# Performance work log

Measured on AMD Instinct MI355X. Metric: run time of the kernel, lower is better.

Reference implementation:

```python
import jax, jax.numpy as jnp
import numpy as np

B, T, D, H = 2, 4096, 768, 12
DH = D // H


def setup_inputs() -> dict:
    key = jax.random.key(0)
    ks = jax.random.split(key, 4)
    x = jax.random.normal(ks[0], (B, T, D), dtype=jnp.float32)
    Wqkv = jax.random.normal(ks[1], (D, 3 * D), dtype=jnp.float32) * (D ** -0.5)
    bqkv = jnp.zeros((3 * D,), dtype=jnp.float32)
    Wproj = jax.random.normal(ks[2], (D, D), dtype=jnp.float32) * (D ** -0.5)
    bproj = jnp.zeros((D,), dtype=jnp.float32)
    return {"x": x, "Wqkv": Wqkv, "bqkv": bqkv, "Wproj": Wproj, "bproj": bproj}


def reference(x, Wqkv, bqkv, Wproj, bproj):
    b, t, c = x.shape
    qkv = x @ Wqkv + bqkv                      # [B,T,3D]
    qkv = qkv.reshape(b, t, H, 3 * DH)
    q, k, v = jnp.split(qkv, 3, axis=-1)       # each [B,T,H,DH]
    q = q.transpose(0, 2, 1, 3)                # [B,H,T,DH]
    k = k.transpose(0, 2, 1, 3)
    v = v.transpose(0, 2, 1, 3)
    att = jnp.einsum('bhqd,bhkd->bhqk', q, k) / (DH ** 0.5)  # [B,H,T,T]
    mask = jnp.tril(jnp.ones((t, t), dtype=bool))
    att = jnp.where(mask, att, jnp.float32(-1e9))
    att = jax.nn.softmax(att, axis=-1)
    out = jnp.einsum('bhqk,bhkd->bhqd', att, v)  # [B,H,T,DH]
    out = out.transpose(0, 2, 1, 3).reshape(b, t, c)
    return out @ Wproj + bproj
```

## Files before the change

kernel.cpp:

```cpp
#include <hip/hip_runtime.h>

typedef unsigned short u16;
typedef unsigned int u32;
typedef __bf16 bf16x8 __attribute__((ext_vector_type(8)));
typedef float f32x4 __attribute__((ext_vector_type(4)));
typedef float f32x16 __attribute__((ext_vector_type(16)));
typedef u16 u16x4 __attribute__((ext_vector_type(4)));
typedef u32 u32x2 __attribute__((ext_vector_type(2)));
typedef u32 u32x4 __attribute__((ext_vector_type(4)));

#define QSCALE 0.18033688011112042f

static __device__ __forceinline__ u16 f2bf(float f) {
  __bf16 h = (__bf16)f;
  return __builtin_bit_cast(u16, h);
}

static __device__ __forceinline__ u32 pk2(float a, float b) {
  return (u32)f2bf(a) | ((u32)f2bf(b) << 16);
}

static __device__ __forceinline__ void gl_lds16(const void* g, void* l) {
  __builtin_amdgcn_global_load_lds(
      (const __attribute__((address_space(1))) unsigned int*)g,
      (__attribute__((address_space(3))) unsigned int*)l, 16, 0, 0);
}

static __device__ __forceinline__ void wait_vmcnt0() {
  asm volatile("s_waitcnt vmcnt(0)" ::: "memory");
  __builtin_amdgcn_sched_barrier(0);
}
static __device__ __forceinline__ void barrier_mem() {
  asm volatile("s_barrier" ::: "memory");
  __builtin_amdgcn_sched_barrier(0);
}

static __device__ __forceinline__ f32x16 zero16() {
  f32x16 z;
#pragma unroll
  for (int i = 0; i < 16; ++i) z[i] = 0.f;
  return z;
}

__global__ void k_cvt(const float* __restrict__ in, u16* __restrict__ out, int n4) {
  int i = blockIdx.x * 256 + threadIdx.x;
  if (i < n4) {
    f32x4 f = ((const f32x4*)in)[i];
    u16x4 u = { f2bf(f[0]), f2bf(f[1]), f2bf(f[2]), f2bf(f[3]) };
    ((u16x4*)out)[i] = u;
  }
}

__global__ void k_transpose_cvt(const float* __restrict__ in, u16* __restrict__ out,
                                int R, int C) {
  __shared__ float tile[32][33];
  const int c0 = blockIdx.x * 32, r0 = blockIdx.y * 32;
  const int tx = threadIdx.x, ty = threadIdx.y;
#pragma unroll
  for (int i = 0; i < 4; ++i)
    tile[ty + i * 8][tx] = in[(size_t)(r0 + ty + i * 8) * C + c0 + tx];
  __syncthreads();
#pragma unroll
  for (int i = 0; i < 4; ++i)
    out[(size_t)(c0 + ty + i * 8) * R + r0 + tx] = f2bf(tile[tx][ty + i * 8]);
}

static __device__ __forceinline__ void gemm_core(const u16* __restrict__ Ag,
                                                 const u16* __restrict__ Btg,
                                                 int K, int m0, int n0,
                                                 u16* As, u16* Bs,
                                                 f32x4 acc[4][4]) {
  const int tid = threadIdx.x;
  const int lane = tid & 63;
  const int wid = tid >> 6;
  const int wm = wid >> 1, wn = wid & 1;
  const int l16 = lane & 15, lg = lane >> 4;

  for (int kt = 0; kt < K; kt += 64) {
    __syncthreads();
#pragma unroll
    for (int i = 0; i < 4; ++i) {
      int chunk = i * 256 + tid;
      int row = chunk >> 3;
      int lcb = ((chunk & 7) << 4) ^ ((row & 7) << 4);
      gl_lds16(Ag + (size_t)(m0 + row) * K + kt + (lcb >> 1),
               As + ((i * 256 + wid * 64) << 3));
    }
#pragma unroll
    for (int i = 0; i < 4; ++i) {
      int chunk = i * 256 + tid;
      int row = chunk >> 3;
      int lcb = ((chunk & 7) << 4) ^ ((row & 7) << 4);
      gl_lds16(Btg + (size_t)(n0 + row) * K + kt + (lcb >> 1),
               Bs + ((i * 256 + wid * 64) << 3));
    }
    __syncthreads();

#pragma unroll
    for (int ks = 0; ks < 2; ++ks) {
      bf16x8 af[4], bfr[4];
#pragma unroll
      for (int mi = 0; mi < 4; ++mi) {
        int row = wm * 64 + mi * 16 + l16;
        int off = row * 128 + ((ks * 64 + (lg << 4)) ^ ((row & 7) << 4));
        af[mi] = *(const bf16x8*)((const char*)As + off);
      }
#pragma unroll
      for (int ni = 0; ni < 4; ++ni) {
        int row = wn * 64 + ni * 16 + l16;
        int off = row * 128 + ((ks * 64 + (lg << 4)) ^ ((row & 7) << 4));
        bfr[ni] = *(const bf16x8*)((const char*)Bs + off);
      }
#pragma unroll
      for (int mi = 0; mi < 4; ++mi)
#pragma unroll
        for (int ni = 0; ni < 4; ++ni)
          acc[mi][ni] = __builtin_amdgcn_mfma_f32_16x16x32_bf16(
              af[mi], bfr[ni], acc[mi][ni], 0, 0, 0);
    }
  }
}

__global__ __launch_bounds__(256) void k_gemm_qkv(
    const u16* __restrict__ A, const u16* __restrict__ Bt,
    const float* __restrict__ bias, u16* __restrict__ Q, u16* __restrict__ Kb,
    u16* __restrict__ Vt) {
  __shared__ __align__(16) u16 As[128 * 64];
  __shared__ __align__(16) u16 Bs[128 * 64];
  const int m0 = blockIdx.y * 128, n0 = blockIdx.x * 128;
  const f32x4 fz = {0.f, 0.f, 0.f, 0.f};
  f32x4 acc[4][4];
#pragma unroll
  for (int mi = 0; mi < 4; ++mi)
#pragma unroll
    for (int ni = 0; ni < 4; ++ni) acc[mi][ni] = fz;

  gemm_core(A, Bt, 768, m0, n0, As, Bs, acc);

  const int tid = threadIdx.x, lane = tid & 63, wid = tid >> 6;
  const int wm = wid >> 1, wn = wid & 1, l16 = lane & 15, lg = lane >> 4;
#pragma unroll
  for (int mi = 0; mi < 4; ++mi)
#pragma unroll
    for (int ni = 0; ni < 4; ++ni) {
      int n = n0 + wn * 64 + ni * 16 + l16;
      float bi = bias[n];
      int h = n / 192;
      int rr = n - h * 192;
      int m0w = m0 + wm * 64 + mi * 16 + lg * 4;
      int bb = m0w >> 12, t0 = m0w & 4095;
      size_t base = ((size_t)(bb * 12 + h) * 4096 + t0) * 64;
      if (rr < 64) {
#pragma unroll
        for (int r = 0; r < 4; ++r)
          Q[base + (size_t)r * 64 + rr] = f2bf((acc[mi][ni][r] + bi) * QSCALE);
      } else if (rr < 128) {
#pragma unroll
        for (int r = 0; r < 4; ++r)
          Kb[base + (size_t)r * 64 + rr - 64] = f2bf(acc[mi][ni][r] + bi);
      } else {
        u16x4 vv;
#pragma unroll
        for (int r = 0; r < 4; ++r) vv[r] = f2bf(acc[mi][ni][r] + bi);
        *(u16x4*)(Vt + ((size_t)(bb * 12 + h) * 64 + (rr - 128)) * 4096 + t0) = vv;
      }
    }
}

__global__ __launch_bounds__(256) void k_gemm_proj(
    const u16* __restrict__ A, const u16* __restrict__ Bt,
    const float* __restrict__ bias, float* __restrict__ out) {
  __shared__ __align__(16) u16 As[128 * 64];
  __shared__ __align__(16) u16 Bs[128 * 64];
  const int m0 = blockIdx.y * 128, n0 = blockIdx.x * 128;
  const f32x4 fz = {0.f, 0.f, 0.f, 0.f};
  f32x4 acc[4][4];
#pragma unroll
  for (int mi = 0; mi < 4; ++mi)
#pragma unroll
    for (int ni = 0; ni < 4; ++ni) acc[mi][ni] = fz;

  gemm_core(A, Bt, 768, m0, n0, As, Bs, acc);

  const int tid = threadIdx.x, lane = tid & 63, wid = tid >> 6;
  const int wm = wid >> 1, wn = wid & 1, l16 = lane & 15, lg = lane >> 4;
#pragma unroll
  for (int mi = 0; mi < 4; ++mi)
#pragma unroll
    for (int ni = 0; ni < 4; ++ni) {
      int n = n0 + wn * 64 + ni * 16 + l16;
      float bi = bias[n];
#pragma unroll
      for (int r = 0; r < 4; ++r) {
        int m = m0 + wm * 64 + mi * 16 + lg * 4 + r;
        out[(size_t)m * 768 + n] = acc[mi][ni][r] + bi;
      }
    }
}

__global__ __launch_bounds__(128) void k_attn(const u16* __restrict__ Qg,
                                              const u16* __restrict__ Kg,
                                              const u16* __restrict__ Vtg,
                                              u16* __restrict__ Og) {
  __shared__ __align__(16) u16 Ks[64 * 64];
  __shared__ __align__(16) u16 Vs[64 * 64];
  const int bid = blockIdx.x;
  const int xcd = bid & 7;
  const int u = bid >> 3;
  const int s = u & 31;
  const int rnd = u >> 5;
  const int bh = xcd * 3 + (rnd >> 1);
  const int jX = (rnd & 1) ? s : (63 - s);
  const int tid = threadIdx.x;
  const int lane = tid & 63;
  const int wid = tid >> 6;
  const int l32 = lane & 31;
  const int hi = lane >> 5;
  const int rxor = (l32 & 7) << 4;
  const size_t qk_base = (size_t)bh * (4096 * 64);
  const size_t vt_base = (size_t)bh * (64 * 4096);
  const int b = bh / 12, h = bh - b * 12;

  const int q0w = jX * 64 + wid * 32;
  const int qrow = q0w + l32;
  const int nkt = jX + 1;

  int coK[4], coVa[4], coVb[4];
#pragma unroll
  for (int st = 0; st < 4; ++st) coK[st] = (st * 32 + hi * 16) ^ rxor;
#pragma unroll
  for (int ks = 0; ks < 4; ++ks) {
    coVa[ks] = (ks * 32 + hi * 8) ^ rxor;
    coVb[ks] = (ks * 32 + 16 + hi * 8) ^ rxor;
  }
  const int rb0 = l32 * 128, rb1 = (32 + l32) * 128;

  const int trow = tid >> 3;
  const int tcol = ((((tid & 7) << 4) ^ ((trow & 7) << 4)) >> 1);
  const int tdst = tid << 3;
  const u16* kp0 = Kg + qk_base + (size_t)trow * 64 + tcol;
  const u16* kp1 = kp0 + (size_t)16 * 64;
  const u16* kp2 = kp0 + (size_t)32 * 64;
  const u16* kp3 = kp0 + (size_t)48 * 64;
  const u16* vq0 = Vtg + vt_base + (size_t)trow * 4096 + tcol;
  const u16* vq1 = vq0 + (size_t)16 * 4096;
  const u16* vq2 = vq0 + (size_t)32 * 4096;
  const u16* vq3 = vq0 + (size_t)48 * 4096;

  auto stage = [&]() {
    gl_lds16(kp0, Ks + tdst);
    gl_lds16(kp1, Ks + 1024 + tdst);
    gl_lds16(kp2, Ks + 2048 + tdst);
    gl_lds16(kp3, Ks + 3072 + tdst);
    gl_lds16(vq0, Vs + tdst);
    gl_lds16(vq1, Vs + 1024 + tdst);
    gl_lds16(vq2, Vs + 2048 + tdst);
    gl_lds16(vq3, Vs + 3072 + tdst);
    kp0 += 4096; kp1 += 4096; kp2 += 4096; kp3 += 4096;
    vq0 += 64; vq1 += 64; vq2 += 64; vq3 += 64;
  };

  bf16x8 qb[4];
#pragma unroll
  for (int st = 0; st < 4; ++st)
    qb[st] = *(const bf16x8*)(Qg + qk_base + (size_t)qrow * 64 + st * 16 + hi * 8);

  f32x16 o0 = zero16(), o1 = zero16();
  float mrun = -3.0e38f, lrun = 0.f;

  for (int kt = 0; kt < nkt; ++kt) {
    stage();
    wait_vmcnt0();
    barrier_mem();

    const bool diag = (kt == nkt - 1);
    const bool halfskip = diag && (wid == 0);
    const char* Kbp = (const char*)Ks;
    const char* Vb = (const char*)Vs;

    f32x16 s0 = zero16(), s1 = zero16();
    __builtin_amdgcn_s_setprio(1);
#pragma unroll
    for (int st = 0; st < 4; ++st) {
      bf16x8 ka0 = *(const bf16x8*)(Kbp + rb0 + coK[st]);
      s0 = __builtin_amdgcn_mfma_f32_32x32x16_bf16(ka0, qb[st], s0, 0, 0, 0);
    }
    if (!halfskip) {
#pragma unroll
      for (int st = 0; st < 4; ++st) {
        bf16x8 ka1 = *(const bf16x8*)(Kbp + rb1 + coK[st]);
        s1 = __builtin_amdgcn_mfma_f32_32x32x16_bf16(ka1, qb[st], s1, 0, 0, 0);
      }
    }
    __builtin_amdgcn_s_setprio(0);

    if (diag) {
      const int kbase = kt * 64 + 4 * hi;
#pragma unroll
      for (int r = 0; r < 16; ++r) {
        int kpv = kbase + (r & 3) + 8 * (r >> 2);
        s0[r] = (kpv > qrow) ? -3.0e38f : s0[r];
        if (!halfskip) s1[r] = (kpv + 32 > qrow) ? -3.0e38f : s1[r];
      }
    }

    float m8[8];
#pragma unroll
    for (int r = 0; r < 8; ++r) {
      float v = fmaxf(s0[r], s0[r + 8]);
      if (!halfskip) v = fmaxf(v, fmaxf(s1[r], s1[r + 8]));
      m8[r] = v;
    }
    float mx = fmaxf(fmaxf(fmaxf(m8[0], m8[1]), fmaxf(m8[2], m8[3])),
                     fmaxf(fmaxf(m8[4], m8[5]), fmaxf(m8[6], m8[7])));
    mx = fmaxf(mx, __shfl_xor(mx, 32, 64));

    if (__ballot(mx > mrun + 8.0f) != 0ull) {
      float mnew = fmaxf(mrun, mx);
      float al = __builtin_amdgcn_exp2f(mrun - mnew);
      o0 *= al;
      o1 *= al;
      lrun *= al;
      mrun = mnew;
    }

#pragma unroll
    for (int r = 0; r < 16; ++r) {
      s0[r] = __builtin_amdgcn_exp2f(s0[r] - mrun);
      if (!halfskip) s1[r] = __builtin_amdgcn_exp2f(s1[r] - mrun);
    }

    float a8[8];
#pragma unroll
    for (int r = 0; r < 8; ++r) {
      float v = s0[r] + s0[r + 8];
      if (!halfskip) v += s1[r] + s1[r + 8];
      a8[r] = v;
    }
    float rs = ((a8[0] + a8[1]) + (a8[2] + a8[3])) +
               ((a8[4] + a8[5]) + (a8[6] + a8[7]));
    rs += __shfl_xor(rs, 32, 64);
    lrun += rs;

    __builtin_amdgcn_s_setprio(1);
#pragma unroll
    for (int ks = 0; ks < 4; ++ks) {
      if (ks >= 2 && halfskip) continue;
      const f32x16& P = (ks >= 2) ? s1 : s0;
      const int base = (ks & 1) * 8;
      u32x4 w = { pk2(P[base + 0], P[base + 1]), pk2(P[base + 2], P[base + 3]),
                  pk2(P[base + 4], P[base + 5]), pk2(P[base + 6], P[base + 7]) };
      bf16x8 pbk = __builtin_bit_cast(bf16x8, w);
      u32x2 q0 = *(const u32x2*)(Vb + rb0 + coVa[ks]);
      u32x2 q1 = *(const u32x2*)(Vb + rb0 + coVb[ks]);
      u32x4 av = {q0[0], q0[1], q1[0], q1[1]};
      bf16x8 va0 = __builtin_bit_cast(bf16x8, av);
      o0 = __builtin_amdgcn_mfma_f32_32x32x16_bf16(va0, pbk, o0, 0, 0, 0);
      u32x2 p0 = *(const u32x2*)(Vb + rb1 + coVa[ks]);
      u32x2 p1 = *(const u32x2*)(Vb + rb1 + coVb[ks]);
      u32x4 bv = {p0[0], p0[1], p1[0], p1[1]};
      bf16x8 va1 = __builtin_bit_cast(bf16x8, bv);
      o1 = __builtin_amdgcn_mfma_f32_32x32x16_bf16(va1, pbk, o1, 0, 0, 0);
    }
    __builtin_amdgcn_s_setprio(0);

    barrier_mem();
  }

  float inv = 1.0f / lrun;
  u16* orow = Og + ((size_t)b * 4096 + qrow) * 768 + h * 64;
#pragma unroll
  for (int gg = 0; gg < 4; ++gg) {
    u16x4 v0, v1;
#pragma unroll
    for (int i = 0; i < 4; ++i) {
      v0[i] = f2bf(o0[4 * gg + i] * inv);
      v1[i] = f2bf(o1[4 * gg + i] * inv);
    }
    *(u16x4*)(orow + 8 * gg + 4 * hi) = v0;
    *(u16x4*)(orow + 32 + 8 * gg + 4 * hi) = v1;
  }
}

extern "C" void kernel_launch(void* const* d_in, const int* in_sizes, int n_in,
                              void* d_out, int out_size, void* d_ws, size_t ws_size,
                              hipStream_t stream) {
  const float* x = (const float*)d_in[0];
  const float* Wqkv = (const float*)d_in[1];
  const float* bqkv = (const float*)d_in[2];
  const float* Wproj = (const float*)d_in[3];
  const float* bproj = (const float*)d_in[4];
  float* out = (float*)d_out;

  char* ws = (char*)d_ws;
  u16* Xbf = (u16*)(ws + 0);
  u16* WqkvT = (u16*)(ws + 12582912);
  u16* WprojT = (u16*)(ws + 16121856);
  u16* Q = (u16*)(ws + 17301504);
  u16* K = (u16*)(ws + 29884416);
  u16* Vt = (u16*)(ws + 42467328);
  u16* O = (u16*)(ws + 55050240);

  k_cvt<<<6144, 256, 0, stream>>>(x, Xbf, 1572864);
  k_transpose_cvt<<<dim3(72, 24), dim3(32, 8), 0, stream>>>(Wqkv, WqkvT, 768, 2304);
  k_transpose_cvt<<<dim3(24, 24), dim3(32, 8), 0, stream>>>(Wproj, WprojT, 768, 768);
  k_gemm_qkv<<<dim3(18, 64), 256, 0, stream>>>(Xbf, WqkvT, bqkv, Q, K, Vt);
  k_attn<<<1536, 128, 0, stream>>>(Q, K, Vt, O);
  k_gemm_proj<<<dim3(6, 64), 256, 0, stream>>>(O, WprojT, bproj, out);
}
```

Baseline: 211.9 us.

## Double-buffer K tiles and defer V wait in attention loop

The attention kernel now keeps two K buffers in shared memory and prefetches the next K tile while the current one is processed. V loading is separated from K, and the wait on V is moved after the QK^T and softmax work, using partial vmcnt waits and an extra barrier. This is meant to hide global-to-LDS load latency behind MFMA and exp work. The cost is more LDS per block and an extra barrier per iteration, which may lower occupancy.

New measurement: 212.9 us. Within noise of the previous version (+0.4%).

```diff
diff --git a/kernel.cpp b/kernel.cpp
--- a/kernel.cpp
+++ b/kernel.cpp
@@ -26,6 +26,14 @@
       (__attribute__((address_space(3))) unsigned int*)l, 16, 0, 0);
 }
 
+static __device__ __forceinline__ void wait_vmcnt8() {
+  asm volatile("s_waitcnt vmcnt(8)" ::: "memory");
+  __builtin_amdgcn_sched_barrier(0);
+}
+static __device__ __forceinline__ void wait_vmcnt4() {
+  asm volatile("s_waitcnt vmcnt(4)" ::: "memory");
+  __builtin_amdgcn_sched_barrier(0);
+}
 static __device__ __forceinline__ void wait_vmcnt0() {
   asm volatile("s_waitcnt vmcnt(0)" ::: "memory");
   __builtin_amdgcn_sched_barrier(0);
@@ -202,7 +210,7 @@
                                               const u16* __restrict__ Kg,
                                               const u16* __restrict__ Vtg,
                                               u16* __restrict__ Og) {
-  __shared__ __align__(16) u16 Ks[64 * 64];
+  __shared__ __align__(16) u16 Ks[2][64 * 64];
   __shared__ __align__(16) u16 Vs[64 * 64];
   const int bid = blockIdx.x;
   const int xcd = bid & 7;
@@ -247,16 +255,18 @@
   const u16* vq2 = vq0 + (size_t)32 * 4096;
   const u16* vq3 = vq0 + (size_t)48 * 4096;
 
-  auto stage = [&]() {
-    gl_lds16(kp0, Ks + tdst);
-    gl_lds16(kp1, Ks + 1024 + tdst);
-    gl_lds16(kp2, Ks + 2048 + tdst);
-    gl_lds16(kp3, Ks + 3072 + tdst);
+  auto stageK = [&](u16* Kd) {
+    gl_lds16(kp0, Kd + tdst);
+    gl_lds16(kp1, Kd + 1024 + tdst);
+    gl_lds16(kp2, Kd + 2048 + tdst);
+    gl_lds16(kp3, Kd + 3072 + tdst);
+    kp0 += 4096; kp1 += 4096; kp2 += 4096; kp3 += 4096;
+  };
+  auto stageV = [&]() {
     gl_lds16(vq0, Vs + tdst);
     gl_lds16(vq1, Vs + 1024 + tdst);
     gl_lds16(vq2, Vs + 2048 + tdst);
     gl_lds16(vq3, Vs + 3072 + tdst);
-    kp0 += 4096; kp1 += 4096; kp2 += 4096; kp3 += 4096;
     vq0 += 64; vq1 += 64; vq2 += 64; vq3 += 64;
   };
 
@@ -268,14 +278,18 @@
   f32x16 o0 = zero16(), o1 = zero16();
   float mrun = -3.0e38f, lrun = 0.f;
 
+  stageK(Ks[0]);
+
   for (int kt = 0; kt < nkt; ++kt) {
-    stage();
-    wait_vmcnt0();
+    const bool more = (kt + 1 < nkt);
+    stageV();
+    if (more) stageK(Ks[(kt + 1) & 1]);
+    if (more) wait_vmcnt8(); else wait_vmcnt4();
     barrier_mem();
 
     const bool diag = (kt == nkt - 1);
     const bool halfskip = diag && (wid == 0);
-    const char* Kbp = (const char*)Ks;
+    const char* Kbp = (const char*)Ks[kt & 1];
     const char* Vb = (const char*)Vs;
 
     f32x16 s0 = zero16(), s1 = zero16();
@@ -341,6 +355,9 @@
                ((a8[4] + a8[5]) + (a8[6] + a8[7]));
     rs += __shfl_xor(rs, 32, 64);
     lrun += rs;
+
+    if (more) wait_vmcnt4(); else wait_vmcnt0();
+    barrier_mem();
 
     __builtin_amdgcn_s_setprio(1);
 #pragma unroll
```
